# Optimization experiments

Hardware: AMD Instinct MI355X
Metric: run time of the kernel (lower is better)

## Reference

```python
import jax, jax.numpy as jnp
import numpy as np

# Model dims (MiniCPM-style decode-only LM inside VoxCPM2)
L, B, D = 16, 4, 1024
H, HD, KVH = 16, 64, 8          # query heads, head dim, KV heads (GQA)
DFF = 4096
S = 2048                         # current KV cache length
SCALE_DEPTH = 1.4                # mup depth scaling
EPS = 1e-5
THETA = 10000.0
W_STD = 0.02


def setup_inputs() -> dict:
    key = jax.random.key(0)
    ks = jax.random.split(key, 12)
    return {
        "inputs_embeds": jax.random.normal(ks[0], (B, D), jnp.float32),
        "k_cache": jax.random.normal(ks[1], (L, B, KVH, S, HD), jnp.float32),
        "v_cache": jax.random.normal(ks[2], (L, B, KVH, S, HD), jnp.float32),
        "ln1_w": jnp.ones((L, D), jnp.float32),
        "ln2_w": jnp.ones((L, D), jnp.float32),
        "norm_w": jnp.ones((D,), jnp.float32),
        "wq": jax.random.normal(ks[3], (L, D, H * HD), jnp.float32) * W_STD,
        "wk": jax.random.normal(ks[4], (L, D, KVH * HD), jnp.float32) * W_STD,
        "wv": jax.random.normal(ks[5], (L, D, KVH * HD), jnp.float32) * W_STD,
        "wo": jax.random.normal(ks[6], (L, H * HD, D), jnp.float32) * W_STD,
        "w_gate": jax.random.normal(ks[7], (L, D, DFF), jnp.float32) * W_STD,
        "w_up": jax.random.normal(ks[8], (L, D, DFF), jnp.float32) * W_STD,
        "w_down": jax.random.normal(ks[9], (L, DFF, D), jnp.float32) * W_STD,
        "cache_length": S,  # position id of the token being decoded
    }


def _rmsnorm(x, w):
    return x * jax.lax.rsqrt(jnp.mean(x * x, axis=-1, keepdims=True) + EPS) * w


def _rotate_half(x):
    x1, x2 = jnp.split(x, 2, axis=-1)
    return jnp.concatenate((-x2, x1), axis=-1)


def _decode_step(inputs_embeds, k_cache, v_cache, ln1_w, ln2_w, norm_w,
                 wq, wk, wv, wo, w_gate, w_up, w_down, cache_length):
    # RoPE tables for the single decode position
    pos = jnp.asarray(cache_length, jnp.float32)
    inv_freq = 1.0 / (THETA ** (jnp.arange(0, HD, 2, dtype=jnp.float32) / HD))
    freqs = pos * inv_freq                       # [HD/2]
    emb = jnp.concatenate((freqs, freqs))        # [HD]
    cos, sin = jnp.cos(emb), jnp.sin(emb)

    mup = SCALE_DEPTH / np.sqrt(L)
    scale = 1.0 / np.sqrt(HD)
    G = H // KVH  # query heads per KV head

    def layer(h, ws):
        l1, l2, Wq, Wk, Wv, Wo, Wg, Wu, Wd, kc, vc = ws
        x = _rmsnorm(h, l1)                                  # [B, D]
        q = (x @ Wq).reshape(B, H, HD)
        k = (x @ Wk).reshape(B, KVH, HD)
        v = (x @ Wv).reshape(B, KVH, HD)
        q = q * cos + _rotate_half(q) * sin
        k = k * cos + _rotate_half(k) * sin
        nk = jnp.concatenate((kc, k[:, :, None, :]), axis=2)  # [B, KVH, S+1, HD]
        nv = jnp.concatenate((vc, v[:, :, None, :]), axis=2)
        qg = q.reshape(B, KVH, G, HD)                         # GQA grouping
        scores = jnp.einsum('bkgd,bksd->bkgs', qg, nk) * scale
        p = jax.nn.softmax(scores, axis=-1)
        o = jnp.einsum('bkgs,bksd->bkgd', p, nv).reshape(B, H * HD)
        h = h + (o @ Wo) * mup                                # mup residual
        x = _rmsnorm(h, l2)
        mlp = (jax.nn.silu(x @ Wg) * (x @ Wu)) @ Wd           # SwiGLU
        h = h + mlp * mup
        return h, (nk, nv)

    h, (next_k, next_v) = jax.lax.scan(
        layer, inputs_embeds,
        (ln1_w, ln2_w, wq, wk, wv, wo, w_gate, w_up, w_down, k_cache, v_cache))
    h = _rmsnorm(h, norm_w)
    return h, next_k, next_v


def reference(inputs_embeds, k_cache, v_cache, ln1_w, ln2_w, norm_w,
              wq, wk, wv, wo, w_gate, w_up, w_down, cache_length):
    h, nk, nv = _decode_step(inputs_embeds, k_cache, v_cache, ln1_w, ln2_w,
                             norm_w, wq, wk, wv, wo, w_gate, w_up, w_down,
                             cache_length)
    return h, nk, nv, jnp.asarray(cache_length + 1, jnp.int64)
```

## Files before the change

### kernel.cpp

```cpp
#include <hip/hip_runtime.h>
#include <math.h>

#define MUP 0.35f
#define SCALE 0.125f
#define EPS 1e-5f

#define WS_HA    0
#define WS_HB    4096
#define WS_YMLP  8192
#define WS_YO    12288
#define WS_QKVP  16384
#define WS_GUP   16384
#define WS_OPART 278528

#define OUT_NK  4096
#define OUT_NV  (4096 + 16*4*8*2049*64)
#define OUT_SC  (4096 + 2*16*4*8*2049*64)

__device__ __forceinline__ float wsum64(float v) {
    v += __shfl_xor(v, 32); v += __shfl_xor(v, 16); v += __shfl_xor(v, 8);
    v += __shfl_xor(v, 4);  v += __shfl_xor(v, 2);  v += __shfl_xor(v, 1);
    return v;
}

__device__ __forceinline__ void fma4(float4& a, float s, const float4 w) {
    a.x = fmaf(s, w.x, a.x); a.y = fmaf(s, w.y, a.y);
    a.z = fmaf(s, w.z, a.z); a.w = fmaf(s, w.w, a.w);
}

__global__ __launch_bounds__(256) void k_init(const float* __restrict__ emb,
                                              const int* __restrict__ cl,
                                              float* __restrict__ ws,
                                              float* __restrict__ out) {
    int tid = threadIdx.x;
    float4* ws4 = (float4*)ws;
    float4 z = {0.f, 0.f, 0.f, 0.f};
    if (blockIdx.x == 0) {
        const float4* e4 = (const float4*)emb;
        #pragma unroll
        for (int k = 0; k < 4; ++k) ws4[(WS_HA >> 2) + k * 256 + tid] = e4[k * 256 + tid];
        if (tid == 0) out[OUT_SC] = (float)(cl[0] + 1);
    } else if (blockIdx.x == 1) {
        #pragma unroll
        for (int k = 0; k < 4; ++k) ws4[(WS_YMLP >> 2) + k * 256 + tid] = z;
    } else {
        #pragma unroll
        for (int k = 0; k < 4; ++k) ws4[(WS_YO >> 2) + k * 256 + tid] = z;
    }
}

__global__ __launch_bounds__(256) void k_a(const float* __restrict__ ln1,
                                           const float* __restrict__ wq,
                                           const float* __restrict__ wk,
                                           const float* __restrict__ wv,
                                           float* __restrict__ ws, int l) {
    float4* ws4 = (float4*)ws;
    int tid = threadIdx.x, w = tid >> 6, lane = tid & 63;
    if (blockIdx.x >= 256) {
        float4 z = {0,0,0,0};
        ws4[(WS_YO >> 2) + (blockIdx.x - 256) * 256 + tid] = z;
        return;
    }
    __shared__ float xs[4][32];
    __shared__ float4 red[4][64][4];
    __shared__ float sred[4][4];
    const int s = blockIdx.x >> 3, xt = blockIdx.x & 7;

    float4 hn[4]; float ss[4];
    #pragma unroll
    for (int b = 0; b < 4; ++b) {
        float4 h = ws4[(WS_HA >> 2) + b * 256 + tid];
        float4 y = ws4[(WS_YMLP >> 2) + b * 256 + tid];
        h.x = fmaf(MUP, y.x, h.x); h.y = fmaf(MUP, y.y, h.y);
        h.z = fmaf(MUP, y.z, h.z); h.w = fmaf(MUP, y.w, h.w);
        hn[b] = h;
        ss[b] = h.x*h.x + h.y*h.y + h.z*h.z + h.w*h.w;
    }
    #pragma unroll
    for (int b = 0; b < 4; ++b) {
        float v = wsum64(ss[b]);
        if (lane == 0) sred[w][b] = v;
    }
    __syncthreads();
    float rstd[4];
    #pragma unroll
    for (int b = 0; b < 4; ++b)
        rstd[b] = rsqrtf((sred[0][b] + sred[1][b] + sred[2][b] + sred[3][b]) * (1.f/1024.f) + EPS);
    if (blockIdx.x == 0) {
        #pragma unroll
        for (int b = 0; b < 4; ++b) ws4[(WS_HB >> 2) + b * 256 + tid] = hn[b];
    }
    {
        int tl = tid - s * 8;
        if (tl >= 0 && tl < 8) {
            float4 g4 = ((const float4*)ln1)[l * 256 + tid];
            #pragma unroll
            for (int b = 0; b < 4; ++b) {
                float4 xv;
                xv.x = hn[b].x * rstd[b] * g4.x; xv.y = hn[b].y * rstd[b] * g4.y;
                xv.z = hn[b].z * rstd[b] * g4.z; xv.w = hn[b].w * rstd[b] * g4.w;
                ((float4*)xs[b])[tl] = xv;
            }
        }
    }
    __syncthreads();

    const float* Wp; int nc, c;
    if (xt < 4)      { Wp = wq + (size_t)l * 1024 * 1024; nc = 1024; c = xt * 256 + lane * 4; }
    else if (xt < 6) { Wp = wk + (size_t)l * 1024 * 512;  nc = 512;  c = (xt - 4) * 256 + lane * 4; }
    else             { Wp = wv + (size_t)l * 1024 * 512;  nc = 512;  c = (xt - 6) * 256 + lane * 4; }
    const float4* W4 = (const float4*)(Wp + c);
    const size_t nc4 = (size_t)(nc >> 2);
    float4 a0 = {0,0,0,0}, a1 = a0, a2 = a0, a3 = a0;
    #pragma unroll
    for (int rr = 0; rr < 8; ++rr) {
        int r = w * 8 + rr;
        float4 wv4 = W4[(size_t)(s * 32 + r) * nc4];
        fma4(a0, xs[0][r], wv4); fma4(a1, xs[1][r], wv4);
        fma4(a2, xs[2][r], wv4); fma4(a3, xs[3][r], wv4);
    }
    red[w][lane][0] = a0; red[w][lane][1] = a1;
    red[w][lane][2] = a2; red[w][lane][3] = a3;
    __syncthreads();
    if (w == 0) {
        float4* QKVP4 = ws4 + (WS_QKVP >> 2);
        #pragma unroll
        for (int b = 0; b < 4; ++b) {
            float4 s0v = red[0][lane][b], s1v = red[1][lane][b],
                   s2v = red[2][lane][b], s3v = red[3][lane][b];
            s0v.x += s1v.x + s2v.x + s3v.x; s0v.y += s1v.y + s2v.y + s3v.y;
            s0v.z += s1v.z + s2v.z + s3v.z; s0v.w += s1v.w + s2v.w + s3v.w;
            QKVP4[(size_t)(s * 4 + b) * 512 + xt * 64 + lane] = s0v;
        }
    }
}

__global__ __launch_bounds__(256) void k_b(const float* __restrict__ kc,
                                           const float* __restrict__ vc,
                                           const int* __restrict__ cl,
                                           float* __restrict__ ws,
                                           float* __restrict__ nk,
                                           float* __restrict__ nv, int l) {
    const int bid = blockIdx.x;
    const int b = bid >> 7, rem = bid & 127, kvh = rem >> 4, c = rem & 15;
    const int s0 = c * 128;
    const int tid = threadIdx.x, w = tid >> 6, lane = tid & 63;
    const int sub = lane >> 4, j = lane & 15;
    float4* ws4 = (float4*)ws;
    const float4* QKVP4 = (const float4*)ws4 + (WS_QKVP >> 2);

    __shared__ float4 vst[128][16];
    __shared__ float sc[2][132];
    __shared__ float wm[2][4];
    __shared__ float oacc[2][4][64];
    __shared__ float wl[2][4];

    const float pos = (float)cl[0];
    float cs4[4], sn4[4];
    #pragma unroll
    for (int m = 0; m < 4; ++m) {
        float t = (float)(4 * (j & 7) + m);
        float fr = pos * __expf(-t * 0.2878231366242557f);
        cs4[m] = cosf(fr); sn4[m] = sinf(fr);
    }
    const float sgn = (j < 8) ? -1.f : 1.f;

    float4 q0 = {0,0,0,0}, q1 = {0,0,0,0};
    #pragma unroll
    for (int sp = 0; sp < 32; ++sp) {
        const float4* qp = QKVP4 + (size_t)(sp * 4 + b) * 512 + kvh * 32;
        float4 t0 = qp[j], t1 = qp[16 + j];
        q0.x += t0.x; q0.y += t0.y; q0.z += t0.z; q0.w += t0.w;
        q1.x += t1.x; q1.y += t1.y; q1.z += t1.z; q1.w += t1.w;
    }
    {
        float4 q0p, q1p;
        q0p.x = __shfl_xor(q0.x, 8); q0p.y = __shfl_xor(q0.y, 8);
        q0p.z = __shfl_xor(q0.z, 8); q0p.w = __shfl_xor(q0.w, 8);
        q1p.x = __shfl_xor(q1.x, 8); q1p.y = __shfl_xor(q1.y, 8);
        q1p.z = __shfl_xor(q1.z, 8); q1p.w = __shfl_xor(q1.w, 8);
        q0.x = q0.x * cs4[0] + sgn * q0p.x * sn4[0];
        q0.y = q0.y * cs4[1] + sgn * q0p.y * sn4[1];
        q0.z = q0.z * cs4[2] + sgn * q0p.z * sn4[2];
        q0.w = q0.w * cs4[3] + sgn * q0p.w * sn4[3];
        q1.x = q1.x * cs4[0] + sgn * q1p.x * sn4[0];
        q1.y = q1.y * cs4[1] + sgn * q1p.y * sn4[1];
        q1.z = q1.z * cs4[2] + sgn * q1p.z * sn4[2];
        q1.w = q1.w * cs4[3] + sgn * q1p.w * sn4[3];
    }

    const size_t cbase = (size_t)((l * 4 + b) * 8 + kvh);
    const float4* kc4 = (const float4*)kc + cbase * 2048 * 16;
    const float4* vc4 = (const float4*)vc + cbase * 2048 * 16;
    float4* nk4 = (float4*)nk + cbase * 2049 * 16;
    float4* nv4 = (float4*)nv + cbase * 2049 * 16;

    float m0 = -1e30f, m1 = -1e30f;
    const int rbase = s0 + w * 32;
    #pragma unroll 4
    for (int i = 0; i < 8; ++i) {
        int r = rbase + i * 4 + sub;
        float4 kv = kc4[(size_t)r * 16 + j];
        float4 vv = vc4[(size_t)r * 16 + j];
        nk4[(size_t)r * 16 + j] = kv;
        nv4[(size_t)r * 16 + j] = vv;
        vst[r - s0][j] = vv;
        float d0 = kv.x*q0.x + kv.y*q0.y + kv.z*q0.z + kv.w*q0.w;
        float d1 = kv.x*q1.x + kv.y*q1.y + kv.z*q1.z + kv.w*q1.w;
        d0 += __shfl_xor(d0, 1); d0 += __shfl_xor(d0, 2);
        d0 += __shfl_xor(d0, 4); d0 += __shfl_xor(d0, 8);
        d1 += __shfl_xor(d1, 1); d1 += __shfl_xor(d1, 2);
        d1 += __shfl_xor(d1, 4); d1 += __shfl_xor(d1, 8);
        d0 *= SCALE; d1 *= SCALE;
        if (j == 0) { sc[0][r - s0] = d0; sc[1][r - s0] = d1; }
        m0 = fmaxf(m0, d0); m1 = fmaxf(m1, d1);
    }
    float4 vnew = {0,0,0,0};
    if (c == 15 && w == 0 && sub == 0) {
        float4 kv = {0,0,0,0};
        #pragma unroll
        for (int sp = 0; sp < 32; ++sp) {
            const float4* pp = QKVP4 + (size_t)(sp * 4 + b) * 512;
            float4 t0 = pp[256 + kvh * 16 + j];
            float4 t1 = pp[384 + kvh * 16 + j];
            kv.x += t0.x; kv.y += t0.y; kv.z += t0.z; kv.w += t0.w;
            vnew.x += t1.x; vnew.y += t1.y; vnew.z += t1.z; vnew.w += t1.w;
        }
        float4 kp;
        kp.x = __shfl_xor(kv.x, 8); kp.y = __shfl_xor(kv.y, 8);
        kp.z = __shfl_xor(kv.z, 8); kp.w = __shfl_xor(kv.w, 8);
        kv.x = kv.x * cs4[0] + sgn * kp.x * sn4[0];
        kv.y = kv.y * cs4[1] + sgn * kp.y * sn4[1];
        kv.z = kv.z * cs4[2] + sgn * kp.z * sn4[2];
        kv.w = kv.w * cs4[3] + sgn * kp.w * sn4[3];
        nk4[(size_t)2048 * 16 + j] = kv;
        nv4[(size_t)2048 * 16 + j] = vnew;
        float d0 = kv.x*q0.x + kv.y*q0.y + kv.z*q0.z + kv.w*q0.w;
        float d1 = kv.x*q1.x + kv.y*q1.y + kv.z*q1.z + kv.w*q1.w;
        d0 += __shfl_xor(d0, 1); d0 += __shfl_xor(d0, 2);
        d0 += __shfl_xor(d0, 4); d0 += __shfl_xor(d0, 8);
        d1 += __shfl_xor(d1, 1); d1 += __shfl_xor(d1, 2);
        d1 += __shfl_xor(d1, 4); d1 += __shfl_xor(d1, 8);
        d0 *= SCALE; d1 *= SCALE;
        if (j == 0) { sc[0][128] = d0; sc[1][128] = d1; }
        m0 = fmaxf(m0, d0); m1 = fmaxf(m1, d1);
    }
    m0 = fmaxf(m0, __shfl_xor(m0, 16)); m0 = fmaxf(m0, __shfl_xor(m0, 32));
    m1 = fmaxf(m1, __shfl_xor(m1, 16)); m1 = fmaxf(m1, __shfl_xor(m1, 32));
    if (lane == 0) { wm[0][w] = m0; wm[1][w] = m1; }
    __syncthreads();
    const float M0 = fmaxf(fmaxf(wm[0][0], wm[0][1]), fmaxf(wm[0][2], wm[0][3]));
    const float M1 = fmaxf(fmaxf(wm[1][0], wm[1][1]), fmaxf(wm[1][2], wm[1][3]));

    float4 o0 = {0,0,0,0}, o1 = {0,0,0,0};
    float l0 = 0.f, l1 = 0.f;
    #pragma unroll 4
    for (int i = 0; i < 8; ++i) {
        int r = rbase + i * 4 + sub;
        float4 vv = vst[r - s0][j];
        float p0 = __expf(sc[0][r - s0] - M0);
        float p1 = __expf(sc[1][r - s0] - M1);
        fma4(o0, p0, vv); fma4(o1, p1, vv);
        l0 += p0; l1 += p1;
    }
    if (c == 15 && w == 0 && sub == 0) {
        float p0 = __expf(sc[0][128] - M0);
        float p1 = __expf(sc[1][128] - M1);
        fma4(o0, p0, vnew); fma4(o1, p1, vnew);
        l0 += p0; l1 += p1;
    }
    o0.x += __shfl_xor(o0.x, 16); o0.x += __shfl_xor(o0.x, 32);
    o0.y += __shfl_xor(o0.y, 16); o0.y += __shfl_xor(o0.y, 32);
    o0.z += __shfl_xor(o0.z, 16); o0.z += __shfl_xor(o0.z, 32);
    o0.w += __shfl_xor(o0.w, 16); o0.w += __shfl_xor(o0.w, 32);
    o1.x += __shfl_xor(o1.x, 16); o1.x += __shfl_xor(o1.x, 32);
    o1.y += __shfl_xor(o1.y, 16); o1.y += __shfl_xor(o1.y, 32);
    o1.z += __shfl_xor(o1.z, 16); o1.z += __shfl_xor(o1.z, 32);
    o1.w += __shfl_xor(o1.w, 16); o1.w += __shfl_xor(o1.w, 32);
    l0 += __shfl_xor(l0, 16); l0 += __shfl_xor(l0, 32);
    l1 += __shfl_xor(l1, 16); l1 += __shfl_xor(l1, 32);
    if (sub == 0) {
        oacc[0][w][4*j+0] = o0.x; oacc[0][w][4*j+1] = o0.y;
        oacc[0][w][4*j+2] = o0.z; oacc[0][w][4*j+3] = o0.w;
        oacc[1][w][4*j+0] = o1.x; oacc[1][w][4*j+1] = o1.y;
        oacc[1][w][4*j+2] = o1.z; oacc[1][w][4*j+3] = o1.w;
    }
    if (lane == 0) { wl[0][w] = l0; wl[1][w] = l1; }
    __syncthreads();
    int pbase = WS_OPART + ((b * 8 + kvh) * 16 + c) * 132;
    if (tid < 128) {
        int h = tid >> 6, d = tid & 63;
        ws[pbase + h * 64 + d] = oacc[h][0][d] + oacc[h][1][d] + oacc[h][2][d] + oacc[h][3][d];
    } else if (tid == 128) {
        ws[pbase + 128] = M0;
        ws[pbase + 129] = wl[0][0] + wl[0][1] + wl[0][2] + wl[0][3];
        ws[pbase + 130] = M1;
        ws[pbase + 131] = wl[1][0] + wl[1][1] + wl[1][2] + wl[1][3];
    }
}

__global__ __launch_bounds__(256) void k_c(const float* __restrict__ wo,
                                           float* __restrict__ ws, int l) {
    float4* ws4 = (float4*)ws;
    int tid = threadIdx.x, w = tid >> 6, lane = tid & 63;
    if (blockIdx.x >= 128) {
        float4 z = {0,0,0,0};
        ws4[(WS_YMLP >> 2) + (blockIdx.x - 128) * 256 + tid] = z;
        return;
    }
    __shared__ float xs[4][32];
    __shared__ float4 red[4][64][4];
    const int xt = blockIdx.x & 3, s = blockIdx.x >> 2;
    if (tid < 128) {
        const int bb = tid >> 5, rr = tid & 31;
        const int r = s * 32 + rr;
        const int kvh = r >> 7, g = (r >> 6) & 1, d = r & 63;
        const float* bp = ws + WS_OPART + (size_t)((bb * 8 + kvh) * 16) * 132;
        float m = -1e30f;
        #pragma unroll
        for (int cc = 0; cc < 16; ++cc)
            m = fmaxf(m, bp[cc * 132 + 128 + 2 * g]);
        float lt = 0.f, ot = 0.f;
        #pragma unroll
        for (int cc = 0; cc < 16; ++cc) {
            float f = __expf(bp[cc * 132 + 128 + 2 * g] - m);
            lt += bp[cc * 132 + 129 + 2 * g] * f;
            ot += bp[cc * 132 + g * 64 + d] * f;
        }
        xs[bb][rr] = ot / lt;
    }
    __syncthreads();
    const float4* W4 = (const float4*)(wo + (size_t)l * 1024 * 1024 + xt * 256 + lane * 4);
    float4 a0 = {0,0,0,0}, a1 = a0, a2 = a0, a3 = a0;
    #pragma unroll
    for (int rr = 0; rr < 8; ++rr) {
        int r = w * 8 + rr;
        float4 wv4 = W4[(size_t)(s * 32 + r) * 256];
        fma4(a0, xs[0][r], wv4); fma4(a1, xs[1][r], wv4);
        fma4(a2, xs[2][r], wv4); fma4(a3, xs[3][r], wv4);
    }
    red[w][lane][0] = a0; red[w][lane][1] = a1;
    red[w][lane][2] = a2; red[w][lane][3] = a3;
    __syncthreads();
    if (w == 0) {
        int c = xt * 256 + lane * 4;
        #pragma unroll
        for (int b = 0; b < 4; ++b) {
            float4 s0v = red[0][lane][b], s1v = red[1][lane][b],
                   s2v = red[2][lane][b], s3v = red[3][lane][b];
            s0v.x += s1v.x + s2v.x + s3v.x; s0v.y += s1v.y + s2v.y + s3v.y;
            s0v.z += s1v.z + s2v.z + s3v.z; s0v.w += s1v.w + s2v.w + s3v.w;
            atomicAdd(&ws[WS_YO + b * 1024 + c + 0], s0v.x);
            atomicAdd(&ws[WS_YO + b * 1024 + c + 1], s0v.y);
            atomicAdd(&ws[WS_YO + b * 1024 + c + 2], s0v.z);
            atomicAdd(&ws[WS_YO + b * 1024 + c + 3], s0v.w);
        }
    }
}

__global__ __launch_bounds__(256) void k_d(const float* __restrict__ ln2,
                                           const float* __restrict__ wg,
                                           const float* __restrict__ wu,
                                           float* __restrict__ ws, int l) {
    float4* ws4 = (float4*)ws;
    int tid = threadIdx.x, w = tid >> 6, lane = tid & 63;
    __shared__ float xs[4][128];
    __shared__ float4 red[4][64][4];
    __shared__ float sred[4][4];
    const int mat = blockIdx.x >> 4, t16 = blockIdx.x & 15, y = blockIdx.y;

    float4 hn[4]; float ss[4];
    #pragma unroll
    for (int b = 0; b < 4; ++b) {
        float4 h = ws4[(WS_HB >> 2) + b * 256 + tid];
        float4 yv = ws4[(WS_YO >> 2) + b * 256 + tid];
        h.x = fmaf(MUP, yv.x, h.x); h.y = fmaf(MUP, yv.y, h.y);
        h.z = fmaf(MUP, yv.z, h.z); h.w = fmaf(MUP, yv.w, h.w);
        hn[b] = h;
        ss[b] = h.x*h.x + h.y*h.y + h.z*h.z + h.w*h.w;
    }
    #pragma unroll
    for (int b = 0; b < 4; ++b) {
        float v = wsum64(ss[b]);
        if (lane == 0) sred[w][b] = v;
    }
    __syncthreads();
    float rstd[4];
    #pragma unroll
    for (int b = 0; b < 4; ++b)
        rstd[b] = rsqrtf((sred[0][b] + sred[1][b] + sred[2][b] + sred[3][b]) * (1.f/1024.f) + EPS);
    if (blockIdx.x == 0 && blockIdx.y == 0) {
        #pragma unroll
        for (int b = 0; b < 4; ++b) ws4[(WS_HA >> 2) + b * 256 + tid] = hn[b];
    }
    {
        int tl = tid - y * 32;
        if (tl >= 0 && tl < 32) {
            float4 g4 = ((const float4*)ln2)[l * 256 + tid];
            #pragma unroll
            for (int b = 0; b < 4; ++b) {
                float4 xv;
                xv.x = hn[b].x * rstd[b] * g4.x; xv.y = hn[b].y * rstd[b] * g4.y;
                xv.z = hn[b].z * rstd[b] * g4.z; xv.w = hn[b].w * rstd[b] * g4.w;
                ((float4*)xs[b])[tl] = xv;
            }
        }
    }
    __syncthreads();

    const float* Wm = (mat ? wu : wg) + (size_t)l * 1024 * 4096;
    const float4* W4 = (const float4*)(Wm + t16 * 256 + lane * 4);
    float4 a0 = {0,0,0,0}, a1 = a0, a2 = a0, a3 = a0;
    #pragma unroll 8
    for (int rr = 0; rr < 32; ++rr) {
        int r = w * 32 + rr;
        float4 wv4 = W4[(size_t)(y * 128 + r) * 1024];
        fma4(a0, xs[0][r], wv4); fma4(a1, xs[1][r], wv4);
        fma4(a2, xs[2][r], wv4); fma4(a3, xs[3][r], wv4);
    }
    red[w][lane][0] = a0; red[w][lane][1] = a1;
    red[w][lane][2] = a2; red[w][lane][3] = a3;
    __syncthreads();
    if (w == 0) {
        float4* GUP4 = ws4 + (WS_GUP >> 2);
        #pragma unroll
        for (int b = 0; b < 4; ++b) {
            float4 s0v = red[0][lane][b], s1v = red[1][lane][b],
                   s2v = red[2][lane][b], s3v = red[3][lane][b];
            s0v.x += s1v.x + s2v.x + s3v.x; s0v.y += s1v.y + s2v.y + s3v.y;
            s0v.z += s1v.z + s2v.z + s3v.z; s0v.w += s1v.w + s2v.w + s3v.w;
            GUP4[(size_t)((mat * 8 + y) * 4 + b) * 1024 + t16 * 64 + lane] = s0v;
        }
    }
}

__global__ __launch_bounds__(256) void k_e(const float* __restrict__ wd,
                                           float* __restrict__ ws, int l) {
    float4* ws4 = (float4*)ws;
    int tid = threadIdx.x, w = tid >> 6, lane = tid & 63;
    __shared__ float ts[4][128];
    __shared__ float4 red[4][64][4];
    const int xt = blockIdx.x, s = blockIdx.y;
    if (tid < 128) {
        const int bb = tid >> 5, i = tid & 31;
        const int f4 = s * 32 + i;
        const float4* GUP4 = (const float4*)ws4 + (WS_GUP >> 2);
        float4 g = {0,0,0,0}, u = {0,0,0,0};
        #pragma unroll
        for (int sp = 0; sp < 8; ++sp) {
            float4 gv = GUP4[(size_t)(sp * 4 + bb) * 1024 + f4];
            float4 uv = GUP4[(size_t)((8 + sp) * 4 + bb) * 1024 + f4];
            g.x += gv.x; g.y += gv.y; g.z += gv.z; g.w += gv.w;
            u.x += uv.x; u.y += uv.y; u.z += uv.z; u.w += uv.w;
        }
        float4 t;
        t.x = (g.x / (1.f + __expf(-g.x))) * u.x;
        t.y = (g.y / (1.f + __expf(-g.y))) * u.y;
        t.z = (g.z / (1.f + __expf(-g.z))) * u.z;
        t.w = (g.w / (1.f + __expf(-g.w))) * u.w;
        ((float4*)ts[bb])[i] = t;
    }
    __syncthreads();
    const float4* W4 = (const float4*)(wd + (size_t)l * 4096 * 1024 + xt * 256 + lane * 4);
    float4 a0 = {0,0,0,0}, a1 = a0, a2 = a0, a3 = a0;
    #pragma unroll 8
    for (int rr = 0; rr < 32; ++rr) {
        int r = w * 32 + rr;
        float4 wv4 = W4[(size_t)(s * 128 + r) * 256];
        fma4(a0, ts[0][r], wv4); fma4(a1, ts[1][r], wv4);
        fma4(a2, ts[2][r], wv4); fma4(a3, ts[3][r], wv4);
    }
    red[w][lane][0] = a0; red[w][lane][1] = a1;
    red[w][lane][2] = a2; red[w][lane][3] = a3;
    __syncthreads();
    if (w == 0) {
        int c = xt * 256 + lane * 4;
        #pragma unroll
        for (int b = 0; b < 4; ++b) {
            float4 s0v = red[0][lane][b], s1v = red[1][lane][b],
                   s2v = red[2][lane][b], s3v = red[3][lane][b];
            s0v.x += s1v.x + s2v.x + s3v.x; s0v.y += s1v.y + s2v.y + s3v.y;
            s0v.z += s1v.z + s2v.z + s3v.z; s0v.w += s1v.w + s2v.w + s3v.w;
            atomicAdd(&ws[WS_YMLP + b * 1024 + c + 0], s0v.x);
            atomicAdd(&ws[WS_YMLP + b * 1024 + c + 1], s0v.y);
            atomicAdd(&ws[WS_YMLP + b * 1024 + c + 2], s0v.z);
            atomicAdd(&ws[WS_YMLP + b * 1024 + c + 3], s0v.w);
        }
    }
}

__global__ __launch_bounds__(256) void k_final(const float* __restrict__ normw,
                                               float* __restrict__ ws,
                                               float* __restrict__ out) {
    float4* ws4 = (float4*)ws;
    int tid = threadIdx.x;
    int b = blockIdx.x, w = tid >> 6, lane = tid & 63;
    __shared__ float sred[4];
    float4 h = ws4[(WS_HA >> 2) + b * 256 + tid];
    float4 y = ws4[(WS_YMLP >> 2) + b * 256 + tid];
    h.x = fmaf(MUP, y.x, h.x); h.y = fmaf(MUP, y.y, h.y);
    h.z = fmaf(MUP, y.z, h.z); h.w = fmaf(MUP, y.w, h.w);
    float ssv = h.x*h.x + h.y*h.y + h.z*h.z + h.w*h.w;
    float v = wsum64(ssv);
    if (lane == 0) sred[w] = v;
    __syncthreads();
    float rstd = rsqrtf((sred[0] + sred[1] + sred[2] + sred[3]) * (1.f/1024.f) + EPS);
    float4 g4 = ((const float4*)normw)[tid];
    float4 o;
    o.x = h.x * rstd * g4.x; o.y = h.y * rstd * g4.y;
    o.z = h.z * rstd * g4.z; o.w = h.w * rstd * g4.w;
    ((float4*)out)[b * 256 + tid] = o;
}

extern "C" void kernel_launch(void* const* d_in, const int* in_sizes, int n_in,
                              void* d_out, int out_size, void* d_ws, size_t ws_size,
                              hipStream_t stream) {
    const float* emb  = (const float*)d_in[0];
    const float* kc   = (const float*)d_in[1];
    const float* vc   = (const float*)d_in[2];
    const float* ln1  = (const float*)d_in[3];
    const float* ln2  = (const float*)d_in[4];
    const float* nrmw = (const float*)d_in[5];
    const float* wq   = (const float*)d_in[6];
    const float* wk   = (const float*)d_in[7];
    const float* wv   = (const float*)d_in[8];
    const float* wo   = (const float*)d_in[9];
    const float* wg   = (const float*)d_in[10];
    const float* wu   = (const float*)d_in[11];
    const float* wd   = (const float*)d_in[12];
    const int*   cl   = (const int*)d_in[13];

    float* out = (float*)d_out;
    float* ws  = (float*)d_ws;
    float* nk  = out + OUT_NK;
    float* nv  = out + OUT_NV;

    k_init<<<3, 256, 0, stream>>>(emb, cl, ws, out);
    for (int l = 0; l < 16; ++l) {
        k_a<<<260, 256, 0, stream>>>(ln1, wq, wk, wv, ws, l);
        k_b<<<512, 256, 0, stream>>>(kc, vc, cl, ws, nk, nv, l);
        k_c<<<132, 256, 0, stream>>>(wo, ws, l);
        k_d<<<dim3(32, 8), 256, 0, stream>>>(ln2, wg, wu, ws, l);
        k_e<<<dim3(4, 32), 256, 0, stream>>>(wd, ws, l);
    }
    k_final<<<4, 256, 0, stream>>>(nrmw, ws, out);
}
```

Baseline: 1.065 ms.

## Double grid sizes for attention and MLP kernels, batch loads up front, use nontemporal cache stores

Splits the KV sequence into 32 chunks of 64 rows instead of 16 of 128, and halves the K-dimension slice per block in the Wo, gate/up and down projections, doubling block counts to raise memory-level parallelism on a bandwidth-bound decode. Weight and KV loads are issued into register arrays before any FMA so more loads are in flight. The KV cache copy uses nontemporal stores to avoid polluting cache. The GUP workspace is moved to its own region, and the down-projection prologue now reduces 16 partials cooperatively across all threads. The cost is more partial-sum traffic and larger reductions.

```diff
diff --git a/kernel.cpp b/kernel.cpp
--- a/kernel.cpp
+++ b/kernel.cpp
@@ -4,14 +4,16 @@
 #define MUP 0.35f
 #define SCALE 0.125f
 #define EPS 1e-5f
+
+typedef float f32x4 __attribute__((ext_vector_type(4)));
 
 #define WS_HA    0
 #define WS_HB    4096
 #define WS_YMLP  8192
 #define WS_YO    12288
 #define WS_QKVP  16384
-#define WS_GUP   16384
 #define WS_OPART 278528
+#define WS_GUP   413696
 
 #define OUT_NK  4096
 #define OUT_NV  (4096 + 16*4*8*2049*64)
@@ -26,6 +28,11 @@
 __device__ __forceinline__ void fma4(float4& a, float s, const float4 w) {
     a.x = fmaf(s, w.x, a.x); a.y = fmaf(s, w.y, a.y);
     a.z = fmaf(s, w.z, a.z); a.w = fmaf(s, w.w, a.w);
+}
+
+__device__ __forceinline__ void nt_store4(const float4 v, float4* p) {
+    f32x4 t = {v.x, v.y, v.z, v.w};
+    __builtin_nontemporal_store(t, (f32x4*)p);
 }
 
 __global__ __launch_bounds__(256) void k_init(const float* __restrict__ emb,
@@ -111,13 +118,16 @@
     else             { Wp = wv + (size_t)l * 1024 * 512;  nc = 512;  c = (xt - 6) * 256 + lane * 4; }
     const float4* W4 = (const float4*)(Wp + c);
     const size_t nc4 = (size_t)(nc >> 2);
+    float4 wr[8];
+    #pragma unroll
+    for (int i = 0; i < 8; ++i)
+        wr[i] = W4[(size_t)(s * 32 + w * 8 + i) * nc4];
     float4 a0 = {0,0,0,0}, a1 = a0, a2 = a0, a3 = a0;
     #pragma unroll
-    for (int rr = 0; rr < 8; ++rr) {
-        int r = w * 8 + rr;
-        float4 wv4 = W4[(size_t)(s * 32 + r) * nc4];
-        fma4(a0, xs[0][r], wv4); fma4(a1, xs[1][r], wv4);
-        fma4(a2, xs[2][r], wv4); fma4(a3, xs[3][r], wv4);
+    for (int i = 0; i < 8; ++i) {
+        int r = w * 8 + i;
+        fma4(a0, xs[0][r], wr[i]); fma4(a1, xs[1][r], wr[i]);
+        fma4(a2, xs[2][r], wr[i]); fma4(a3, xs[3][r], wr[i]);
     }
     red[w][lane][0] = a0; red[w][lane][1] = a1;
     red[w][lane][2] = a2; red[w][lane][3] = a3;
@@ -142,15 +152,15 @@
                                            float* __restrict__ nk,
                                            float* __restrict__ nv, int l) {
     const int bid = blockIdx.x;
-    const int b = bid >> 7, rem = bid & 127, kvh = rem >> 4, c = rem & 15;
-    const int s0 = c * 128;
+    const int b = bid >> 8, kvh = (bid >> 5) & 7, c = bid & 31;
+    const int s0 = c * 64;
     const int tid = threadIdx.x, w = tid >> 6, lane = tid & 63;
     const int sub = lane >> 4, j = lane & 15;
     float4* ws4 = (float4*)ws;
     const float4* QKVP4 = (const float4*)ws4 + (WS_QKVP >> 2);
 
-    __shared__ float4 vst[128][16];
-    __shared__ float sc[2][132];
+    __shared__ float4 vst[64][16];
+    __shared__ float sc[2][68];
     __shared__ float wm[2][4];
     __shared__ float oacc[2][4][64];
     __shared__ float wl[2][4];
@@ -166,7 +176,7 @@
     const float sgn = (j < 8) ? -1.f : 1.f;
 
     float4 q0 = {0,0,0,0}, q1 = {0,0,0,0};
-    #pragma unroll
+    #pragma unroll 8
     for (int sp = 0; sp < 32; ++sp) {
         const float4* qp = QKVP4 + (size_t)(sp * 4 + b) * 512 + kvh * 32;
         float4 t0 = qp[j], t1 = qp[16 + j];
@@ -195,16 +205,26 @@
     float4* nk4 = (float4*)nk + cbase * 2049 * 16;
     float4* nv4 = (float4*)nv + cbase * 2049 * 16;
 
+    const int rbase = s0 + w * 16;
+    float4 kr[4], vr[4];
+    #pragma unroll
+    for (int i = 0; i < 4; ++i) {
+        int r = rbase + i * 4 + sub;
+        kr[i] = kc4[(size_t)r * 16 + j];
+        vr[i] = vc4[(size_t)r * 16 + j];
+    }
+    #pragma unroll
+    for (int i = 0; i < 4; ++i) {
+        int r = rbase + i * 4 + sub;
+        nt_store4(kr[i], &nk4[(size_t)r * 16 + j]);
+        nt_store4(vr[i], &nv4[(size_t)r * 16 + j]);
+        vst[r - s0][j] = vr[i];
+    }
     float m0 = -1e30f, m1 = -1e30f;
-    const int rbase = s0 + w * 32;
-    #pragma unroll 4
-    for (int i = 0; i < 8; ++i) {
+    #pragma unroll
+    for (int i = 0; i < 4; ++i) {
         int r = rbase + i * 4 + sub;
-        float4 kv = kc4[(size_t)r * 16 + j];
-        float4 vv = vc4[(size_t)r * 16 + j];
-        nk4[(size_t)r * 16 + j] = kv;
-        nv4[(size_t)r * 16 + j] = vv;
-        vst[r - s0][j] = vv;
+        float4 kv = kr[i];
         float d0 = kv.x*q0.x + kv.y*q0.y + kv.z*q0.z + kv.w*q0.w;
         float d1 = kv.x*q1.x + kv.y*q1.y + kv.z*q1.z + kv.w*q1.w;
         d0 += __shfl_xor(d0, 1); d0 += __shfl_xor(d0, 2);
@@ -216,9 +236,9 @@
         m0 = fmaxf(m0, d0); m1 = fmaxf(m1, d1);
     }
     float4 vnew = {0,0,0,0};
-    if (c == 15 && w == 0 && sub == 0) {
+    if (c == 31 && w == 0 && sub == 0) {
         float4 kv = {0,0,0,0};
-        #pragma unroll
+        #pragma unroll 8
         for (int sp = 0; sp < 32; ++sp) {
             const float4* pp = QKVP4 + (size_t)(sp * 4 + b) * 512;
             float4 t0 = pp[256 + kvh * 16 + j];
@@ -242,7 +262,7 @@
         d1 += __shfl_xor(d1, 1); d1 += __shfl_xor(d1, 2);
         d1 += __shfl_xor(d1, 4); d1 += __shfl_xor(d1, 8);
         d0 *= SCALE; d1 *= SCALE;
-        if (j == 0) { sc[0][128] = d0; sc[1][128] = d1; }
+        if (j == 0) { sc[0][64] = d0; sc[1][64] = d1; }
         m0 = fmaxf(m0, d0); m1 = fmaxf(m1, d1);
     }
     m0 = fmaxf(m0, __shfl_xor(m0, 16)); m0 = fmaxf(m0, __shfl_xor(m0, 32));
@@ -254,8 +274,8 @@
 
     float4 o0 = {0,0,0,0}, o1 = {0,0,0,0};
     float l0 = 0.f, l1 = 0.f;
-    #pragma unroll 4
-    for (int i = 0; i < 8; ++i) {
+    #pragma unroll
+    for (int i = 0; i < 4; ++i) {
         int r = rbase + i * 4 + sub;
         float4 vv = vst[r - s0][j];
         float p0 = __expf(sc[0][r - s0] - M0);
@@ -263,9 +283,9 @@
         fma4(o0, p0, vv); fma4(o1, p1, vv);
         l0 += p0; l1 += p1;
     }
-    if (c == 15 && w == 0 && sub == 0) {
-        float p0 = __expf(sc[0][128] - M0);
-        float p1 = __expf(sc[1][128] - M1);
+    if (c == 31 && w == 0 && sub == 0) {
+        float p0 = __expf(sc[0][64] - M0);
+        float p1 = __expf(sc[1][64] - M1);
         fma4(o0, p0, vnew); fma4(o1, p1, vnew);
         l0 += p0; l1 += p1;
     }
@@ -287,7 +307,7 @@
     }
     if (lane == 0) { wl[0][w] = l0; wl[1][w] = l1; }
     __syncthreads();
-    int pbase = WS_OPART + ((b * 8 + kvh) * 16 + c) * 132;
+    int pbase = WS_OPART + ((b * 8 + kvh) * 32 + c) * 132;
     if (tid < 128) {
         int h = tid >> 6, d = tid & 63;
         ws[pbase + h * 64 + d] = oacc[h][0][d] + oacc[h][1][d] + oacc[h][2][d] + oacc[h][3][d];
@@ -303,26 +323,26 @@
                                            float* __restrict__ ws, int l) {
     float4* ws4 = (float4*)ws;
     int tid = threadIdx.x, w = tid >> 6, lane = tid & 63;
-    if (blockIdx.x >= 128) {
+    if (blockIdx.x >= 256) {
         float4 z = {0,0,0,0};
-        ws4[(WS_YMLP >> 2) + (blockIdx.x - 128) * 256 + tid] = z;
+        ws4[(WS_YMLP >> 2) + (blockIdx.x - 256) * 256 + tid] = z;
         return;
     }
-    __shared__ float xs[4][32];
+    __shared__ float xs[4][16];
     __shared__ float4 red[4][64][4];
     const int xt = blockIdx.x & 3, s = blockIdx.x >> 2;
-    if (tid < 128) {
-        const int bb = tid >> 5, rr = tid & 31;
-        const int r = s * 32 + rr;
+    if (tid < 64) {
+        const int bb = tid >> 4, rr = tid & 15;
+        const int r = s * 16 + rr;
         const int kvh = r >> 7, g = (r >> 6) & 1, d = r & 63;
-        const float* bp = ws + WS_OPART + (size_t)((bb * 8 + kvh) * 16) * 132;
+        const float* bp = ws + WS_OPART + (size_t)((bb * 8 + kvh) * 32) * 132;
         float m = -1e30f;
-        #pragma unroll
-        for (int cc = 0; cc < 16; ++cc)
+        #pragma unroll 8
+        for (int cc = 0; cc < 32; ++cc)
             m = fmaxf(m, bp[cc * 132 + 128 + 2 * g]);
         float lt = 0.f, ot = 0.f;
-        #pragma unroll
-        for (int cc = 0; cc < 16; ++cc) {
+        #pragma unroll 8
+        for (int cc = 0; cc < 32; ++cc) {
             float f = __expf(bp[cc * 132 + 128 + 2 * g] - m);
             lt += bp[cc * 132 + 129 + 2 * g] * f;
             ot += bp[cc * 132 + g * 64 + d] * f;
@@ -331,13 +351,16 @@
     }
     __syncthreads();
     const float4* W4 = (const float4*)(wo + (size_t)l * 1024 * 1024 + xt * 256 + lane * 4);
+    float4 wr[4];
+    #pragma unroll
+    for (int i = 0; i < 4; ++i)
+        wr[i] = W4[(size_t)(s * 16 + w * 4 + i) * 256];
     float4 a0 = {0,0,0,0}, a1 = a0, a2 = a0, a3 = a0;
     #pragma unroll
-    for (int rr = 0; rr < 8; ++rr) {
-        int r = w * 8 + rr;
-        float4 wv4 = W4[(size_t)(s * 32 + r) * 256];
-        fma4(a0, xs[0][r], wv4); fma4(a1, xs[1][r], wv4);
-        fma4(a2, xs[2][r], wv4); fma4(a3, xs[3][r], wv4);
+    for (int i = 0; i < 4; ++i) {
+        int r = w * 4 + i;
+        fma4(a0, xs[0][r], wr[i]); fma4(a1, xs[1][r], wr[i]);
+        fma4(a2, xs[2][r], wr[i]); fma4(a3, xs[3][r], wr[i]);
     }
     red[w][lane][0] = a0; red[w][lane][1] = a1;
     red[w][lane][2] = a2; red[w][lane][3] = a3;
@@ -364,7 +387,7 @@
                                            float* __restrict__ ws, int l) {
     float4* ws4 = (float4*)ws;
     int tid = threadIdx.x, w = tid >> 6, lane = tid & 63;
-    __shared__ float xs[4][128];
+    __shared__ float xs[4][64];
     __shared__ float4 red[4][64][4];
     __shared__ float sred[4][4];
     const int mat = blockIdx.x >> 4, t16 = blockIdx.x & 15, y = blockIdx.y;
@@ -394,8 +417,8 @@
         for (int b = 0; b < 4; ++b) ws4[(WS_HA >> 2) + b * 256 + tid] = hn[b];
     }
     {
-        int tl = tid - y * 32;
-        if (tl >= 0 && tl < 32) {
+        int tl = tid - y * 16;
+        if (tl >= 0 && tl < 16) {
             float4 g4 = ((const float4*)ln2)[l * 256 + tid];
             #pragma unroll
             for (int b = 0; b < 4; ++b) {
@@ -410,13 +433,16 @@
 
     const float* Wm = (mat ? wu : wg) + (size_t)l * 1024 * 4096;
     const float4* W4 = (const float4*)(Wm + t16 * 256 + lane * 4);
+    float4 wr[16];
+    #pragma unroll
+    for (int i = 0; i < 16; ++i)
+        wr[i] = W4[(size_t)(y * 64 + w * 16 + i) * 1024];
     float4 a0 = {0,0,0,0}, a1 = a0, a2 = a0, a3 = a0;
-    #pragma unroll 8
-    for (int rr = 0; rr < 32; ++rr) {
-        int r = w * 32 + rr;
-        float4 wv4 = W4[(size_t)(y * 128 + r) * 1024];
-        fma4(a0, xs[0][r], wv4); fma4(a1, xs[1][r], wv4);
-        fma4(a2, xs[2][r], wv4); fma4(a3, xs[3][r], wv4);
+    #pragma unroll
+    for (int i = 0; i < 16; ++i) {
+        int r = w * 16 + i;
+        fma4(a0, xs[0][r], wr[i]); fma4(a1, xs[1][r], wr[i]);
+        fma4(a2, xs[2][r], wr[i]); fma4(a3, xs[3][r], wr[i]);
     }
     red[w][lane][0] = a0; red[w][lane][1] = a1;
     red[w][lane][2] = a2; red[w][lane][3] = a3;
@@ -429,7 +455,7 @@
                    s2v = red[2][lane][b], s3v = red[3][lane][b];
             s0v.x += s1v.x + s2v.x + s3v.x; s0v.y += s1v.y + s2v.y + s3v.y;
             s0v.z += s1v.z + s2v.z + s3v.z; s0v.w += s1v.w + s2v.w + s3v.w;
-            GUP4[(size_t)((mat * 8 + y) * 4 + b) * 1024 + t16 * 64 + lane] = s0v;
+            GUP4[(size_t)((mat * 16 + y) * 4 + b) * 1024 + t16 * 64 + lane] = s0v;
         }
     }
 }
@@ -438,18 +464,32 @@
                                            float* __restrict__ ws, int l) {
     float4* ws4 = (float4*)ws;
     int tid = threadIdx.x, w = tid >> 6, lane = tid & 63;
-    __shared__ float ts[4][128];
+    __shared__ float ts[4][64];
+    __shared__ float4 gp[4][16][4], up_[4][16][4];
     __shared__ float4 red[4][64][4];
     const int xt = blockIdx.x, s = blockIdx.y;
-    if (tid < 128) {
-        const int bb = tid >> 5, i = tid & 31;
-        const int f4 = s * 32 + i;
+    {
         const float4* GUP4 = (const float4*)ws4 + (WS_GUP >> 2);
+        const int bb = tid >> 6, c4 = (tid >> 2) & 15, spg = tid & 3;
+        const int f4 = s * 16 + c4;
         float4 g = {0,0,0,0}, u = {0,0,0,0};
         #pragma unroll
-        for (int sp = 0; sp < 8; ++sp) {
+        for (int k = 0; k < 4; ++k) {
+            int sp = spg * 4 + k;
             float4 gv = GUP4[(size_t)(sp * 4 + bb) * 1024 + f4];
-            float4 uv = GUP4[(size_t)((8 + sp) * 4 + bb) * 1024 + f4];
+            float4 uv = GUP4[(size_t)((16 + sp) * 4 + bb) * 1024 + f4];
+            g.x += gv.x; g.y += gv.y; g.z += gv.z; g.w += gv.w;
+            u.x += uv.x; u.y += uv.y; u.z += uv.z; u.w += uv.w;
+        }
+        gp[bb][c4][spg] = g; up_[bb][c4][spg] = u;
+    }
+    __syncthreads();
+    if (tid < 64) {
+        const int bb = tid >> 4, c4 = tid & 15;
+        float4 g = gp[bb][c4][0], u = up_[bb][c4][0];
+        #pragma unroll
+        for (int k = 1; k < 4; ++k) {
+            float4 gv = gp[bb][c4][k], uv = up_[bb][c4][k];
             g.x += gv.x; g.y += gv.y; g.z += gv.z; g.w += gv.w;
             u.x += uv.x; u.y += uv.y; u.z += uv.z; u.w += uv.w;
         }
@@ -458,17 +498,20 @@
         t.y = (g.y / (1.f + __expf(-g.y))) * u.y;
         t.z = (g.z / (1.f + __expf(-g.z))) * u.z;
         t.w = (g.w / (1.f + __expf(-g.w))) * u.w;
-        ((float4*)ts[bb])[i] = t;
+        ((float4*)ts[bb])[c4] = t;
     }
     __syncthreads();
     const float4* W4 = (const float4*)(wd + (size_t)l * 4096 * 1024 + xt * 256 + lane * 4);
+    float4 wr[16];
+    #pragma unroll
+    for (int i = 0; i < 16; ++i)
+        wr[i] = W4[(size_t)(s * 64 + w * 16 + i) * 256];
     float4 a0 = {0,0,0,0}, a1 = a0, a2 = a0, a3 = a0;
-    #pragma unroll 8
-    for (int rr = 0; rr < 32; ++rr) {
-        int r = w * 32 + rr;
-        float4 wv4 = W4[(size_t)(s * 128 + r) * 256];
-        fma4(a0, ts[0][r], wv4); fma4(a1, ts[1][r], wv4);
-        fma4(a2, ts[2][r], wv4); fma4(a3, ts[3][r], wv4);
+    #pragma unroll
+    for (int i = 0; i < 16; ++i) {
+        int r = w * 16 + i;
+        fma4(a0, ts[0][r], wr[i]); fma4(a1, ts[1][r], wr[i]);
+        fma4(a2, ts[2][r], wr[i]); fma4(a3, ts[3][r], wr[i]);
     }
     red[w][lane][0] = a0; red[w][lane][1] = a1;
     red[w][lane][2] = a2; red[w][lane][3] = a3;
@@ -538,10 +581,10 @@
     k_init<<<3, 256, 0, stream>>>(emb, cl, ws, out);
     for (int l = 0; l < 16; ++l) {
         k_a<<<260, 256, 0, stream>>>(ln1, wq, wk, wv, ws, l);
-        k_b<<<512, 256, 0, stream>>>(kc, vc, cl, ws, nk, nv, l);
-        k_c<<<132, 256, 0, stream>>>(wo, ws, l);
-        k_d<<<dim3(32, 8), 256, 0, stream>>>(ln2, wg, wu, ws, l);
-        k_e<<<dim3(4, 32), 256, 0, stream>>>(wd, ws, l);
+        k_b<<<1024, 256, 0, stream>>>(kc, vc, cl, ws, nk, nv, l);
+        k_c<<<260, 256, 0, stream>>>(wo, ws, l);
+        k_d<<<dim3(32, 16), 256, 0, stream>>>(ln2, wg, wu, ws, l);
+        k_e<<<dim3(4, 64), 256, 0, stream>>>(wd, ws, l);
     }
     k_final<<<4, 256, 0, stream>>>(nrmw, ws, out);
 }
```

After: 1.215 ms. +14.1%, slower.
